# Kernel tuning notes

Hardware: AMD Instinct MI355X
Metric: run time of the kernel (lower is better)

## Reference

```python
import jax, jax.numpy as jnp
import numpy as np

EMBED = 1024
HEAD = 128

def setup_inputs() -> dict:
    key = jax.random.key(0)
    k1, k2, k3, k4 = jax.random.split(key, 4)
    x = jax.random.normal(k1, (8, 2048, EMBED), dtype=jnp.float32)
    s = 1.0 / np.sqrt(EMBED)
    Wk = jax.random.normal(k2, (EMBED, HEAD), dtype=jnp.float32) * s
    Wq = jax.random.normal(k3, (EMBED, HEAD), dtype=jnp.float32) * s
    Wv = jax.random.normal(k4, (EMBED, HEAD), dtype=jnp.float32) * s
    return {"x": x, "Wk": Wk, "Wq": Wq, "Wv": Wv}

def reference(x, Wk, Wq, Wv):
    # x: [B,T,E]; projections: [B,T,H]
    k = x @ Wk
    q = x @ Wq
    v = x @ Wv
    T = x.shape[1]
    # NOTE: original scales by 1/sqrt(embedding_size), not head_size
    scale = 1.0 / jnp.sqrt(jnp.asarray(EMBED, dtype=x.dtype))
    scores = jnp.einsum('bth,bsh->bts', q, k) * scale  # [B,T,T]
    causal = jnp.tril(jnp.ones((T, T), dtype=bool))
    scores = jnp.where(causal, scores, -jnp.inf)
    attn = jax.nn.softmax(scores, axis=-1)
    return jnp.einsum('bts,bsh->bth', attn, v)
```

## Files before the change

kernel.cpp:

```cpp
#include <hip/hip_runtime.h>
#include <math.h>

typedef short bf16x2 __attribute__((ext_vector_type(2)));
typedef short bf16x4 __attribute__((ext_vector_type(4)));
typedef short bf16x8 __attribute__((ext_vector_type(8)));
typedef float f32x4 __attribute__((ext_vector_type(4)));

#define EMBED 1024
#define HEAD 128
#define BATCH 8
#define SEQ 2048

__device__ __forceinline__ short f2bf(float f) {
  union { float f; unsigned u; } v;
  v.f = f;
  unsigned r = v.u + 0x7fffu + ((v.u >> 16) & 1u);
  return (short)(r >> 16);
}

__device__ __forceinline__ void async_copy16(const void* g, void* l) {
#if __has_builtin(__builtin_amdgcn_global_load_lds)
  __builtin_amdgcn_global_load_lds(
      (const __attribute__((address_space(1))) unsigned int*)g,
      (__attribute__((address_space(3))) unsigned int*)l, 16, 0, 0);
#else
  *(f32x4*)l = *(const f32x4*)g;
#endif
}

__global__ __launch_bounds__(256) void wtrans_kernel(
    const float* __restrict__ Wq, const float* __restrict__ Wk,
    const float* __restrict__ Wv, short* __restrict__ WT) {
  __shared__ float tile[32][33];
  int kt = blockIdx.x * 32;
  int ht = blockIdx.y * 32;
  int mtx = blockIdx.z;
  const float* W = (mtx == 0) ? Wq : ((mtx == 1) ? Wk : Wv);
  float scale = (mtx == 0) ? (1.4426950408889634f / 32.0f) : 1.0f;
  int tc = threadIdx.x & 31;
  int tr = threadIdx.x >> 5;
#pragma unroll
  for (int i = 0; i < 4; i++) {
    int r = tr + i * 8;
    tile[r][tc] = W[(size_t)(kt + r) * HEAD + ht + tc];
  }
  __syncthreads();
#pragma unroll
  for (int i = 0; i < 4; i++) {
    int r = tr + i * 8;
    WT[(size_t)(mtx * HEAD + ht + r) * EMBED + kt + tc] = f2bf(tile[tc][r] * scale);
  }
}

__global__ __launch_bounds__(256, 3) void proj_kernel(
    const float* __restrict__ x, const short* __restrict__ WT,
    short* __restrict__ q, short* __restrict__ k, short* __restrict__ vT) {
  __shared__ __align__(16) short As[2][64 * 72];
  __shared__ __align__(16) short Bs[2][64 * 128];
  int tid = threadIdx.x;
  int w = tid >> 6, lane = tid & 63, quad = lane >> 4, sub = lane & 15;
  int mw = w & 1, nw = w >> 1;
  int bx = blockIdx.x;
  int nt = bx % 3;
  int mt = bx / 3;
  int m0 = mt * 64;
  int bb = m0 >> 11;
  int t0 = m0 & 2047;

  int arow = tid >> 2;
  int akq = (tid & 3) * 16;
  const float* xbase = x + (size_t)(m0 + arow) * EMBED + akq;
  int aoff = arow * 72 + akq;

  const short* wsrc[4];
#pragma unroll
  for (int j = 0; j < 4; j++) {
    int cc = j * 256 + tid;
    wsrc[j] = WT + (size_t)(nt * 128 + (cc & 127)) * EMBED + (cc >> 7) * 8;
  }

  f32x4 acc[2][4];
#pragma unroll
  for (int am = 0; am < 2; am++)
#pragma unroll
    for (int an = 0; an < 4; an++) acc[am][an] = (f32x4)(0.0f);

  {
    f32x4 x0 = *(const f32x4*)(xbase + 0);
    f32x4 x1 = *(const f32x4*)(xbase + 4);
    f32x4 x2 = *(const f32x4*)(xbase + 8);
    f32x4 x3 = *(const f32x4*)(xbase + 12);
    bf16x8 w0, w1;
    w0[0]=f2bf(x0[0]); w0[1]=f2bf(x0[1]); w0[2]=f2bf(x0[2]); w0[3]=f2bf(x0[3]);
    w0[4]=f2bf(x1[0]); w0[5]=f2bf(x1[1]); w0[6]=f2bf(x1[2]); w0[7]=f2bf(x1[3]);
    w1[0]=f2bf(x2[0]); w1[1]=f2bf(x2[1]); w1[2]=f2bf(x2[2]); w1[3]=f2bf(x2[3]);
    w1[4]=f2bf(x3[0]); w1[5]=f2bf(x3[1]); w1[6]=f2bf(x3[2]); w1[7]=f2bf(x3[3]);
    *(bf16x8*)&As[0][aoff] = w0;
    *(bf16x8*)&As[0][aoff + 8] = w1;
#pragma unroll
    for (int j = 0; j < 4; j++) async_copy16(wsrc[j], &Bs[0][(j * 256 + tid) * 8]);
  }
  f32x4 xr0 = *(const f32x4*)(xbase + 64);
  f32x4 xr1 = *(const f32x4*)(xbase + 68);
  f32x4 xr2 = *(const f32x4*)(xbase + 72);
  f32x4 xr3 = *(const f32x4*)(xbase + 76);

  for (int it = 0; it < 16; it++) {
    int cur = it & 1;
    __syncthreads();
    if (it < 15) {
      int nxt = cur ^ 1;
      bf16x8 w0, w1;
      w0[0]=f2bf(xr0[0]); w0[1]=f2bf(xr0[1]); w0[2]=f2bf(xr0[2]); w0[3]=f2bf(xr0[3]);
      w0[4]=f2bf(xr1[0]); w0[5]=f2bf(xr1[1]); w0[6]=f2bf(xr1[2]); w0[7]=f2bf(xr1[3]);
      w1[0]=f2bf(xr2[0]); w1[1]=f2bf(xr2[1]); w1[2]=f2bf(xr2[2]); w1[3]=f2bf(xr2[3]);
      w1[4]=f2bf(xr3[0]); w1[5]=f2bf(xr3[1]); w1[6]=f2bf(xr3[2]); w1[7]=f2bf(xr3[3]);
      *(bf16x8*)&As[nxt][aoff] = w0;
      *(bf16x8*)&As[nxt][aoff + 8] = w1;
      int kb1 = (it + 1) * 64;
#pragma unroll
      for (int j = 0; j < 4; j++)
        async_copy16(wsrc[j] + kb1, &Bs[nxt][(j * 256 + tid) * 8]);
      if (it < 14) {
        int kb2 = (it + 2) * 64;
        xr0 = *(const f32x4*)(xbase + kb2);
        xr1 = *(const f32x4*)(xbase + kb2 + 4);
        xr2 = *(const f32x4*)(xbase + kb2 + 8);
        xr3 = *(const f32x4*)(xbase + kb2 + 12);
      }
    }
#pragma unroll
    for (int ks = 0; ks < 2; ks++) {
      bf16x8 a0 = *(const bf16x8*)&As[cur][(mw * 32 + sub) * 72 + ks * 32 + quad * 8];
      bf16x8 a1 = *(const bf16x8*)&As[cur][(mw * 32 + 16 + sub) * 72 + ks * 32 + quad * 8];
#pragma unroll
      for (int an = 0; an < 4; an++) {
        bf16x8 bb = *(const bf16x8*)&Bs[cur][((ks * 4 + quad) * 128 + nw * 64 + an * 16 + sub) * 8];
        acc[0][an] = __builtin_amdgcn_mfma_f32_16x16x32_bf16(a0, bb, acc[0][an], 0, 0, 0);
        acc[1][an] = __builtin_amdgcn_mfma_f32_16x16x32_bf16(a1, bb, acc[1][an], 0, 0, 0);
      }
    }
  }

  if (nt < 2) {
    short* dst = (nt == 0) ? q : k;
#pragma unroll
    for (int am = 0; am < 2; am++)
#pragma unroll
      for (int an = 0; an < 4; an++) {
        int col = nw * 64 + an * 16 + sub;
#pragma unroll
        for (int r = 0; r < 4; r++) {
          int m = m0 + mw * 32 + am * 16 + quad * 4 + r;
          dst[(size_t)m * HEAD + col] = f2bf(acc[am][an][r]);
        }
      }
  } else {
    short* vls = &As[0][0];
    __syncthreads();
#pragma unroll
    for (int am = 0; am < 2; am++)
#pragma unroll
      for (int an = 0; an < 4; an++) {
        int h = nw * 64 + an * 16 + sub;
        int m = mw * 32 + am * 16 + quad * 4;
        bf16x4 pv;
#pragma unroll
        for (int r = 0; r < 4; r++) pv[r] = f2bf(acc[am][an][r]);
        *(bf16x4*)&vls[h * 72 + m] = pv;
      }
    __syncthreads();
    int h = tid >> 1, seg = tid & 1;
    bf16x8 v0 = *(const bf16x8*)&vls[h * 72 + seg * 32];
    bf16x8 v1 = *(const bf16x8*)&vls[h * 72 + seg * 32 + 8];
    bf16x8 v2 = *(const bf16x8*)&vls[h * 72 + seg * 32 + 16];
    bf16x8 v3 = *(const bf16x8*)&vls[h * 72 + seg * 32 + 24];
    short* dp = vT + (size_t)(bb * HEAD + h) * SEQ + t0 + seg * 32;
    *(bf16x8*)(dp) = v0;
    *(bf16x8*)(dp + 8) = v1;
    *(bf16x8*)(dp + 16) = v2;
    *(bf16x8*)(dp + 24) = v3;
  }
}

__global__ __launch_bounds__(256, 4) void attn_kernel(
    const short* __restrict__ q, const short* __restrict__ k,
    const short* __restrict__ vT, float* __restrict__ o_acc,
    float* __restrict__ l_acc) {
  __shared__ __align__(16) short Kb[2][4096];
  __shared__ __align__(16) short Vb[2][4096];
  __shared__ __align__(16) short Pb[4][2][16 * 40];
  int tid = threadIdx.x;
  int w = tid >> 6, lane = tid & 63, quad = lane >> 4, sub = lane & 15;
  int bx = blockIdx.x;
  int b = bx & 7;
  int v = 79 - (bx >> 3);
  int qt, c;
  if (v < 8)       { qt = v;                               c = 0; }
  else if (v < 24) { int i2 = v - 8;  qt = 8  + (i2 >> 1); c = i2 & 1; }
  else if (v < 48) { int i2 = v - 24; qt = 16 + i2 / 3;    c = i2 % 3; }
  else             { int i2 = v - 48; qt = 24 + (i2 >> 2); c = i2 & 3; }
  int q0 = qt * 64;
  int kb0 = c * 512;
  int len = min(512, q0 + 64 - kb0);
  int ntiles = len >> 5;

  const short* kp = k + (size_t)b * SEQ * HEAD;
  const short* vp = vT + (size_t)b * HEAD * SEQ;
  int cc0 = tid, cc1 = tid + 256;

  bf16x8 qf[4];
  const short* qrow = q + (size_t)(b * SEQ + q0 + w * 16 + sub) * HEAD + quad * 8;
#pragma unroll
  for (int kc = 0; kc < 4; kc++) qf[kc] = *(const bf16x8*)(qrow + kc * 32);

  f32x4 o[8];
#pragma unroll
  for (int h = 0; h < 8; h++) o[h] = (f32x4)(0.0f);
  float l[4] = {0.0f, 0.0f, 0.0f, 0.0f};
  int wrow = q0 + w * 16;
  int qrq = wrow + quad * 4;

  async_copy16(kp + (size_t)(kb0 + (cc0 & 31)) * HEAD + (cc0 >> 5) * 8, &Kb[0][cc0 * 8]);
  async_copy16(kp + (size_t)(kb0 + (cc1 & 31)) * HEAD + (cc1 >> 5) * 8, &Kb[0][cc1 * 8]);
  async_copy16(vp + (size_t)(cc0 & 127) * SEQ + kb0 + (cc0 >> 7) * 8, &Vb[0][cc0 * 8]);
  async_copy16(vp + (size_t)(cc1 & 127) * SEQ + kb0 + (cc1 >> 7) * 8, &Vb[0][cc1 * 8]);

  for (int j = 0; j < ntiles; j++) {
    int kb = kb0 + j * 32;
    int cur = j & 1;
    __syncthreads();
    if (j + 1 < ntiles) {
      int nxt = cur ^ 1;
      int kb1 = kb + 32;
      async_copy16(kp + (size_t)(kb1 + (cc0 & 31)) * HEAD + (cc0 >> 5) * 8, &Kb[nxt][cc0 * 8]);
      async_copy16(kp + (size_t)(kb1 + (cc1 & 31)) * HEAD + (cc1 >> 5) * 8, &Kb[nxt][cc1 * 8]);
      async_copy16(vp + (size_t)(cc0 & 127) * SEQ + kb1 + (cc0 >> 7) * 8, &Vb[nxt][cc0 * 8]);
      async_copy16(vp + (size_t)(cc1 & 127) * SEQ + kb1 + (cc1 >> 7) * 8, &Vb[nxt][cc1 * 8]);
    }
    f32x4 s0 = (f32x4)(0.0f), s1 = (f32x4)(0.0f);
#pragma unroll
    for (int kk = 0; kk < 4; kk++) {
      bf16x8 f0 = *(const bf16x8*)&Kb[cur][((kk * 4 + quad) * 32 + sub) * 8];
      bf16x8 f1 = *(const bf16x8*)&Kb[cur][((kk * 4 + quad) * 32 + 16 + sub) * 8];
      s0 = __builtin_amdgcn_mfma_f32_16x16x32_bf16(qf[kk], f0, s0, 0, 0, 0);
      s1 = __builtin_amdgcn_mfma_f32_16x16x32_bf16(qf[kk], f1, s1, 0, 0, 0);
    }
    bool edge = (kb + 31 > wrow);
    float e0[4], e1[4];
#pragma unroll
    for (int r = 0; r < 4; r++) {
      e0[r] = __builtin_amdgcn_exp2f(s0[r]);
      e1[r] = __builtin_amdgcn_exp2f(s1[r]);
    }
    if (edge) {
#pragma unroll
      for (int r = 0; r < 4; r++) {
        if (kb + sub > qrq + r) e0[r] = 0.0f;
        if (kb + 16 + sub > qrq + r) e1[r] = 0.0f;
      }
    }
    short* pw = &Pb[w][cur][0];
#pragma unroll
    for (int r = 0; r < 4; r++) {
      l[r] += e0[r] + e1[r];
      pw[(quad * 4 + r) * 40 + sub] = f2bf(e0[r]);
      pw[(quad * 4 + r) * 40 + sub + 16] = f2bf(e1[r]);
    }
    bf16x8 pa = *(const bf16x8*)&pw[sub * 40 + quad * 8];
#pragma unroll
    for (int h8 = 0; h8 < 8; h8++) {
      bf16x8 vf = *(const bf16x8*)&Vb[cur][(quad * 128 + h8 * 16 + sub) * 8];
      o[h8] = __builtin_amdgcn_mfma_f32_16x16x32_bf16(pa, vf, o[h8], 0, 0, 0);
    }
  }

  float* ob = o_acc + (size_t)(b * SEQ + qrq) * HEAD + sub;
#pragma unroll
  for (int r = 0; r < 4; r++)
#pragma unroll
    for (int h8 = 0; h8 < 8; h8++)
      unsafeAtomicAdd(ob + (size_t)r * HEAD + h8 * 16, o[h8][r]);
#pragma unroll
  for (int r = 0; r < 4; r++) {
#pragma unroll
    for (int off = 1; off < 16; off <<= 1) l[r] += __shfl_xor(l[r], off);
  }
  if (sub == 0) {
#pragma unroll
    for (int r = 0; r < 4; r++)
      unsafeAtomicAdd(&l_acc[b * SEQ + qrq + r], l[r]);
  }
}

__global__ __launch_bounds__(256) void norm_kernel(
    float* __restrict__ o, const float* __restrict__ l_acc) {
  int idx = blockIdx.x * 256 + threadIdx.x;
  f32x4 v = ((const f32x4*)o)[idx];
  float inv = 1.0f / l_acc[idx >> 5];
  v[0] *= inv; v[1] *= inv; v[2] *= inv; v[3] *= inv;
  ((f32x4*)o)[idx] = v;
}

extern "C" void kernel_launch(void* const* d_in, const int* in_sizes, int n_in,
                              void* d_out, int out_size, void* d_ws, size_t ws_size,
                              hipStream_t stream) {
  const float* x  = (const float*)d_in[0];
  const float* Wk = (const float*)d_in[1];
  const float* Wq = (const float*)d_in[2];
  const float* Wv = (const float*)d_in[3];
  char* ws = (char*)d_ws;
  short* WT    = (short*)(ws);
  short* vT    = (short*)(ws + (size_t)1  * (1 << 20));
  short* q     = (short*)(ws + (size_t)5  * (1 << 20));
  short* k     = (short*)(ws + (size_t)9  * (1 << 20));
  float* l_acc = (float*)(ws + (size_t)13 * (1 << 20));
  float* out   = (float*)d_out;

  hipMemsetAsync(out, 0, (size_t)BATCH * SEQ * HEAD * sizeof(float), stream);
  hipMemsetAsync(l_acc, 0, (size_t)BATCH * SEQ * sizeof(float), stream);
  wtrans_kernel<<<dim3(32, 4, 3), 256, 0, stream>>>(Wq, Wk, Wv, WT);
  proj_kernel<<<dim3(768), 256, 0, stream>>>(x, WT, q, k, vT);
  attn_kernel<<<dim3(640), 256, 0, stream>>>(q, k, vT, out, l_acc);
  norm_kernel<<<dim3(2048), 256, 0, stream>>>(out, l_acc);
}
```

Baseline: 178.0 us.

## Fuse Q/K/V projections into one block per row tile to reuse x

The projection kernel now has each block compute all three Q, K and V outputs (384 columns) for a 64-row tile, using 512 threads, instead of launching three blocks per row tile. The x tile is loaded from global memory and converted to bf16 only once instead of three times, which cuts redundant fp32 reads of the largest input. In exchange the blocks are larger, use more LDS and registers, and there are only 256 of them, which may lower occupancy and load balance across CUs.

```diff
diff --git a/kernel.cpp b/kernel.cpp
--- a/kernel.cpp
+++ b/kernel.cpp
@@ -52,81 +52,74 @@
   }
 }
 
-__global__ __launch_bounds__(256, 3) void proj_kernel(
+__global__ __launch_bounds__(512, 2) void proj_kernel(
     const float* __restrict__ x, const short* __restrict__ WT,
     short* __restrict__ q, short* __restrict__ k, short* __restrict__ vT) {
   __shared__ __align__(16) short As[2][64 * 72];
-  __shared__ __align__(16) short Bs[2][64 * 128];
+  __shared__ __align__(16) short Bs[2][3072 * 8];
   int tid = threadIdx.x;
   int w = tid >> 6, lane = tid & 63, quad = lane >> 4, sub = lane & 15;
   int mw = w & 1, nw = w >> 1;
-  int bx = blockIdx.x;
-  int nt = bx % 3;
-  int mt = bx / 3;
+  int mt = blockIdx.x;
   int m0 = mt * 64;
   int bb = m0 >> 11;
   int t0 = m0 & 2047;
 
-  int arow = tid >> 2;
-  int akq = (tid & 3) * 16;
+  int arow = tid >> 3;
+  int akq = (tid & 7) * 8;
   const float* xbase = x + (size_t)(m0 + arow) * EMBED + akq;
   int aoff = arow * 72 + akq;
 
-  const short* wsrc[4];
-#pragma unroll
-  for (int j = 0; j < 4; j++) {
-    int cc = j * 256 + tid;
-    wsrc[j] = WT + (size_t)(nt * 128 + (cc & 127)) * EMBED + (cc >> 7) * 8;
-  }
-
-  f32x4 acc[2][4];
+  int kcg = tid >> 7;
+  int n0 = tid & 127;
+  const short* wsrc[6];
+  int bdst[6];
+#pragma unroll
+  for (int j = 0; j < 3; j++)
+#pragma unroll
+    for (int kk = 0; kk < 2; kk++) {
+      int kc = kcg * 2 + kk;
+      int n = j * 128 + n0;
+      wsrc[j * 2 + kk] = WT + (size_t)n * EMBED + kc * 8;
+      bdst[j * 2 + kk] = (kc * 384 + n) * 8;
+    }
+
+  f32x4 acc[2][6];
 #pragma unroll
   for (int am = 0; am < 2; am++)
 #pragma unroll
-    for (int an = 0; an < 4; an++) acc[am][an] = (f32x4)(0.0f);
+    for (int an = 0; an < 6; an++) acc[am][an] = (f32x4)(0.0f);
 
   {
     f32x4 x0 = *(const f32x4*)(xbase + 0);
     f32x4 x1 = *(const f32x4*)(xbase + 4);
-    f32x4 x2 = *(const f32x4*)(xbase + 8);
-    f32x4 x3 = *(const f32x4*)(xbase + 12);
-    bf16x8 w0, w1;
+    bf16x8 w0;
     w0[0]=f2bf(x0[0]); w0[1]=f2bf(x0[1]); w0[2]=f2bf(x0[2]); w0[3]=f2bf(x0[3]);
     w0[4]=f2bf(x1[0]); w0[5]=f2bf(x1[1]); w0[6]=f2bf(x1[2]); w0[7]=f2bf(x1[3]);
-    w1[0]=f2bf(x2[0]); w1[1]=f2bf(x2[1]); w1[2]=f2bf(x2[2]); w1[3]=f2bf(x2[3]);
-    w1[4]=f2bf(x3[0]); w1[5]=f2bf(x3[1]); w1[6]=f2bf(x3[2]); w1[7]=f2bf(x3[3]);
     *(bf16x8*)&As[0][aoff] = w0;
-    *(bf16x8*)&As[0][aoff + 8] = w1;
-#pragma unroll
-    for (int j = 0; j < 4; j++) async_copy16(wsrc[j], &Bs[0][(j * 256 + tid) * 8]);
+#pragma unroll
+    for (int j = 0; j < 6; j++) async_copy16(wsrc[j], &Bs[0][bdst[j]]);
   }
   f32x4 xr0 = *(const f32x4*)(xbase + 64);
   f32x4 xr1 = *(const f32x4*)(xbase + 68);
-  f32x4 xr2 = *(const f32x4*)(xbase + 72);
-  f32x4 xr3 = *(const f32x4*)(xbase + 76);
 
   for (int it = 0; it < 16; it++) {
     int cur = it & 1;
     __syncthreads();
     if (it < 15) {
       int nxt = cur ^ 1;
-      bf16x8 w0, w1;
+      bf16x8 w0;
       w0[0]=f2bf(xr0[0]); w0[1]=f2bf(xr0[1]); w0[2]=f2bf(xr0[2]); w0[3]=f2bf(xr0[3]);
       w0[4]=f2bf(xr1[0]); w0[5]=f2bf(xr1[1]); w0[6]=f2bf(xr1[2]); w0[7]=f2bf(xr1[3]);
-      w1[0]=f2bf(xr2[0]); w1[1]=f2bf(xr2[1]); w1[2]=f2bf(xr2[2]); w1[3]=f2bf(xr2[3]);
-      w1[4]=f2bf(xr3[0]); w1[5]=f2bf(xr3[1]); w1[6]=f2bf(xr3[2]); w1[7]=f2bf(xr3[3]);
       *(bf16x8*)&As[nxt][aoff] = w0;
-      *(bf16x8*)&As[nxt][aoff + 8] = w1;
       int kb1 = (it + 1) * 64;
 #pragma unroll
-      for (int j = 0; j < 4; j++)
-        async_copy16(wsrc[j] + kb1, &Bs[nxt][(j * 256 + tid) * 8]);
+      for (int j = 0; j < 6; j++)
+        async_copy16(wsrc[j] + kb1, &Bs[nxt][bdst[j]]);
       if (it < 14) {
         int kb2 = (it + 2) * 64;
         xr0 = *(const f32x4*)(xbase + kb2);
         xr1 = *(const f32x4*)(xbase + kb2 + 4);
-        xr2 = *(const f32x4*)(xbase + kb2 + 8);
-        xr3 = *(const f32x4*)(xbase + kb2 + 12);
       }
     }
 #pragma unroll
@@ -134,53 +127,45 @@
       bf16x8 a0 = *(const bf16x8*)&As[cur][(mw * 32 + sub) * 72 + ks * 32 + quad * 8];
       bf16x8 a1 = *(const bf16x8*)&As[cur][(mw * 32 + 16 + sub) * 72 + ks * 32 + quad * 8];
 #pragma unroll
-      for (int an = 0; an < 4; an++) {
-        bf16x8 bb = *(const bf16x8*)&Bs[cur][((ks * 4 + quad) * 128 + nw * 64 + an * 16 + sub) * 8];
-        acc[0][an] = __builtin_amdgcn_mfma_f32_16x16x32_bf16(a0, bb, acc[0][an], 0, 0, 0);
-        acc[1][an] = __builtin_amdgcn_mfma_f32_16x16x32_bf16(a1, bb, acc[1][an], 0, 0, 0);
+      for (int an = 0; an < 6; an++) {
+        bf16x8 bf = *(const bf16x8*)&Bs[cur][((ks * 4 + quad) * 384 + nw * 96 + an * 16 + sub) * 8];
+        acc[0][an] = __builtin_amdgcn_mfma_f32_16x16x32_bf16(a0, bf, acc[0][an], 0, 0, 0);
+        acc[1][an] = __builtin_amdgcn_mfma_f32_16x16x32_bf16(a1, bf, acc[1][an], 0, 0, 0);
       }
     }
   }
 
-  if (nt < 2) {
-    short* dst = (nt == 0) ? q : k;
-#pragma unroll
-    for (int am = 0; am < 2; am++)
-#pragma unroll
-      for (int an = 0; an < 4; an++) {
-        int col = nw * 64 + an * 16 + sub;
+  __syncthreads();
+  short* vls = &As[0][0];
+#pragma unroll
+  for (int am = 0; am < 2; am++)
+#pragma unroll
+    for (int an = 0; an < 6; an++) {
+      int g = nw * 6 + an;
+      int mtx = g >> 3;
+      int colm = (g & 7) * 16 + sub;
+      if (mtx < 2) {
+        short* dst = (mtx == 0) ? q : k;
 #pragma unroll
         for (int r = 0; r < 4; r++) {
           int m = m0 + mw * 32 + am * 16 + quad * 4 + r;
-          dst[(size_t)m * HEAD + col] = f2bf(acc[am][an][r]);
+          dst[(size_t)m * HEAD + colm] = f2bf(acc[am][an][r]);
         }
+      } else {
+        int mm = mw * 32 + am * 16 + quad * 4;
+        bf16x4 pv;
+#pragma unroll
+        for (int r = 0; r < 4; r++) pv[r] = f2bf(acc[am][an][r]);
+        *(bf16x4*)&vls[colm * 72 + mm] = pv;
       }
-  } else {
-    short* vls = &As[0][0];
-    __syncthreads();
-#pragma unroll
-    for (int am = 0; am < 2; am++)
-#pragma unroll
-      for (int an = 0; an < 4; an++) {
-        int h = nw * 64 + an * 16 + sub;
-        int m = mw * 32 + am * 16 + quad * 4;
-        bf16x4 pv;
-#pragma unroll
-        for (int r = 0; r < 4; r++) pv[r] = f2bf(acc[am][an][r]);
-        *(bf16x4*)&vls[h * 72 + m] = pv;
-      }
-    __syncthreads();
-    int h = tid >> 1, seg = tid & 1;
-    bf16x8 v0 = *(const bf16x8*)&vls[h * 72 + seg * 32];
-    bf16x8 v1 = *(const bf16x8*)&vls[h * 72 + seg * 32 + 8];
-    bf16x8 v2 = *(const bf16x8*)&vls[h * 72 + seg * 32 + 16];
-    bf16x8 v3 = *(const bf16x8*)&vls[h * 72 + seg * 32 + 24];
-    short* dp = vT + (size_t)(bb * HEAD + h) * SEQ + t0 + seg * 32;
-    *(bf16x8*)(dp) = v0;
-    *(bf16x8*)(dp + 8) = v1;
-    *(bf16x8*)(dp + 16) = v2;
-    *(bf16x8*)(dp + 24) = v3;
-  }
+    }
+  __syncthreads();
+  int h = tid >> 2, seg = tid & 3;
+  bf16x8 v0 = *(const bf16x8*)&vls[h * 72 + seg * 16];
+  bf16x8 v1 = *(const bf16x8*)&vls[h * 72 + seg * 16 + 8];
+  short* dp = vT + (size_t)(bb * HEAD + h) * SEQ + t0 + seg * 16;
+  *(bf16x8*)(dp) = v0;
+  *(bf16x8*)(dp + 8) = v1;
 }
 
 __global__ __launch_bounds__(256, 4) void attn_kernel(
@@ -320,7 +305,7 @@
   hipMemsetAsync(out, 0, (size_t)BATCH * SEQ * HEAD * sizeof(float), stream);
   hipMemsetAsync(l_acc, 0, (size_t)BATCH * SEQ * sizeof(float), stream);
   wtrans_kernel<<<dim3(32, 4, 3), 256, 0, stream>>>(Wq, Wk, Wv, WT);
-  proj_kernel<<<dim3(768), 256, 0, stream>>>(x, WT, q, k, vT);
+  proj_kernel<<<dim3(256), 512, 0, stream>>>(x, WT, q, k, vT);
   attn_kernel<<<dim3(640), 256, 0, stream>>>(q, k, vT, out, l_acc);
   norm_kernel<<<dim3(2048), 256, 0, stream>>>(out, l_acc);
 }
```

Result: no change. 175.6 us (-1.3%).
